# Optimization experiments

Measured on AMD Instinct MI355X. Metric: run time of the kernel, lower is better.

## Reference

```python
import jax, jax.numpy as jnp
import numpy as np
from jax import lax

B, T, C = 2, 4096, 2048
HD = 64            # args.head_size == full wkv dim here
H = 1              # num_wkv_heads (forced to 1 by time_faaaa reshape)
D = HD // H        # per-head dim
LAYER, NL = 12, 24
DMIX, DDEC = 32, 64


def setup_inputs() -> dict:
    key = jax.random.key(0)
    ks = jax.random.split(key, 12)
    r01 = LAYER / (NL - 1)          # ratio_0_to_1
    r10 = 1.0 - LAYER / NL          # ratio_1_to_almost0
    ddd = (np.arange(C, dtype=np.float64) / C)
    f32 = np.float32
    maa = lambda p: (1.0 - ddd ** p).astype(f32).reshape(1, 1, C)
    time_maa_x = jnp.asarray(maa(r10))
    time_maa_w = jnp.asarray(maa(r10))
    time_maa_k = jnp.asarray(maa(r10))
    time_maa_v = jnp.asarray((1.0 - (ddd ** r10 + 0.3 * r01)).astype(f32).reshape(1, 1, C))
    time_maa_r = jnp.asarray(maa(0.5 * r10))
    time_maa_g = jnp.asarray(maa(0.5 * r10))
    n = np.arange(HD, dtype=np.float64)
    decay_speed = (-6.0 + 5.0 * (n / (HD - 1)) ** (0.7 + 1.3 * r01)).astype(f32)
    time_decay = jnp.asarray(decay_speed.reshape(1, 1, HD))
    zig = ((np.arange(HD) + 1) % 3 - 1) * 0.1
    time_faaaa = jnp.asarray((r01 * (1.0 - n / (HD - 1)) + zig).astype(f32).reshape(H, D))
    u = lambda k, sh, s=0.01: jax.random.uniform(k, sh, jnp.float32, -s, s)
    time_maa_w1 = u(ks[0], (C, DMIX * 5))
    time_maa_w2 = u(ks[1], (5, DMIX, C))
    time_decay_w1 = u(ks[2], (C, DDEC))
    time_decay_w2 = u(ks[3], (DDEC, HD))
    W_r = jax.random.normal(ks[4], (C, HD), jnp.float32) * 0.02
    W_k = jax.random.normal(ks[5], (C, HD), jnp.float32) * 0.02
    W_v = jax.random.normal(ks[6], (C, HD), jnp.float32) * 0.02
    W_g = jax.random.normal(ks[7], (C, HD), jnp.float32) * 0.02
    W_o = jax.random.normal(ks[8], (HD, C), jnp.float32) * 0.02
    hidden_states = jax.random.normal(ks[9], (B, T, C), jnp.float32)
    shift_state = jax.random.normal(ks[10], (B, C), jnp.float32)
    wkv_state = jax.random.normal(ks[11], (B, H, D, D), jnp.float32)
    return dict(hidden_states=hidden_states, shift_state=shift_state, wkv_state=wkv_state,
                time_maa_x=time_maa_x, time_maa_w=time_maa_w, time_maa_k=time_maa_k,
                time_maa_v=time_maa_v, time_maa_r=time_maa_r, time_maa_g=time_maa_g,
                time_maa_w1=time_maa_w1, time_maa_w2=time_maa_w2,
                time_decay=time_decay, time_decay_w1=time_decay_w1, time_decay_w2=time_decay_w2,
                time_faaaa=time_faaaa, W_r=W_r, W_k=W_k, W_v=W_v, W_g=W_g, W_o=W_o)


def reference(hidden_states, shift_state, wkv_state,
              time_maa_x, time_maa_w, time_maa_k, time_maa_v, time_maa_r, time_maa_g,
              time_maa_w1, time_maa_w2, time_decay, time_decay_w1, time_decay_w2,
              time_faaaa, W_r, W_k, W_v, W_g, W_o):
    hs = hidden_states
    # token shift: prepend shift_state, drop last token, take delta
    xx = jnp.concatenate([shift_state[:, None, :], hs[:, :-1]], axis=1) - hs  # (B,T,C)
    lx = hs[:, -1]
    # LoRA token-shift mixing
    xxx = hs + xx * time_maa_x
    xxx = jnp.tanh(xxx @ time_maa_w1).reshape(B, T, 5, DMIX)
    m = jnp.einsum('btfd,fdc->fbtc', xxx, time_maa_w2)  # (5,B,T,C)
    mw, mk, mv, mr, mg = m[0], m[1], m[2], m[3], m[4]
    xw = hs + xx * (time_maa_w + mw)
    xk = hs + xx * (time_maa_k + mk)
    xv = hs + xx * (time_maa_v + mv)
    xr = hs + xx * (time_maa_r + mr)
    xg = hs + xx * (time_maa_g + mg)
    r = xr @ W_r                                  # (B,T,HD)
    k = xk @ W_k
    v = xv @ W_v
    g = jax.nn.silu(xg @ W_g)
    w = time_decay + jnp.tanh(xw @ time_decay_w1) @ time_decay_w2  # (B,T,HD)
    logw = -jnp.exp(w)                            # log of per-channel decay
    # heads: (B,T,H,D) -> time-major (T,B,H,D) for scan
    tm = lambda x: jnp.moveaxis(x.reshape(B, T, H, D), 1, 0)
    rs, ks_, vs, ws = tm(r), tm(k), tm(v), tm(logw)
    u = time_faaaa[None, :, :, None]              # (1,H,D,1) broadcast over key dim

    def step(s, inp):
        rt, kt, vt, wt = inp                      # each (B,H,D)
        kv = kt[..., :, None] * vt[..., None, :]  # (B,H,Dk,Dv)
        ot = jnp.einsum('bhk,bhkv->bhv', rt, s + u * kv)
        s = s * jnp.exp(wt)[..., None] + kv
        return s, ot

    s_final, o = lax.scan(step, wkv_state, (rs, ks_, vs, ws))
    o = jnp.moveaxis(o, 0, 1).reshape(B, T, H * D)  # (B,T,HD)
    out = (o * g) @ W_o                             # (B,T,C)
    return out, lx, s_final
```

## Files before the change

kernel.cpp:

```cpp
#include <hip/hip_runtime.h>

#define TB 2
#define TT 4096
#define TC 2048
#define TM 8192
#define THD 64
#define TNCH 64

typedef __attribute__((ext_vector_type(8))) short bf16x8;
typedef __attribute__((ext_vector_type(4))) float f32x4;

__device__ __forceinline__ float us2f(unsigned short u){
    union { unsigned int u; float f; } x; x.u = ((unsigned int)u) << 16; return x.f;
}
__device__ __forceinline__ unsigned short f2us(float f){
    unsigned int u = __float_as_uint(f);
    unsigned int r = (u + 0x7fffu + ((u >> 16) & 1u)) >> 16;
    return (unsigned short)r;
}

__global__ void k_cvt(const float* __restrict__ src, unsigned short* __restrict__ dst, int n4){
    int i = blockIdx.x * 256 + threadIdx.x;
    if (i < n4){
        float4 v = *(const float4*)(src + (size_t)i * 4);
        ushort4 u; u.x = f2us(v.x); u.y = f2us(v.y); u.z = f2us(v.z); u.w = f2us(v.w);
        *(ushort4*)(dst + (size_t)i * 4) = u;
    }
}

__global__ void k_cvt5t(const float* __restrict__ s0, const float* __restrict__ s1,
                        const float* __restrict__ s2, const float* __restrict__ s3,
                        const float* __restrict__ s4, unsigned short* __restrict__ Wblk){
    __shared__ float T[64][65];
    int tid = threadIdx.x;
    int mat = blockIdx.y, c0 = blockIdx.x * 64;
    const float* s = (mat == 0) ? s0 : (mat == 1) ? s1 : (mat == 2) ? s2 : (mat == 3) ? s3 : s4;
#pragma unroll
    for (int i = 0; i < 4; ++i){
        int idx = i * 256 + tid;
        int cc = idx >> 4, g = idx & 15;
        float4 v = *(const float4*)(s + (size_t)(c0 + cc) * 64 + g * 4);
        T[cc][g * 4 + 0] = v.x; T[cc][g * 4 + 1] = v.y;
        T[cc][g * 4 + 2] = v.z; T[cc][g * 4 + 3] = v.w;
    }
    __syncthreads();
    size_t base = ((size_t)mat * 32 + (c0 >> 6)) * 4096;
#pragma unroll
    for (int i = 0; i < 4; ++i){
        int idx = i * 256 + tid;
        int h = idx >> 4, g = idx & 15;
        ushort4 u;
        u.x = f2us(T[g * 4 + 0][h]); u.y = f2us(T[g * 4 + 1][h]);
        u.z = f2us(T[g * 4 + 2][h]); u.w = f2us(T[g * 4 + 3][h]);
        *(ushort4*)(Wblk + base + (size_t)h * 64 + g * 4) = u;
    }
}

__global__ void k_lx(const float* __restrict__ hs, float* __restrict__ o){
    int i = blockIdx.x * 256 + threadIdx.x;
    if (i < TB * TC){
        int b = i >> 11, c = i & (TC - 1);
        o[i] = hs[((size_t)(b * TT + TT - 1)) * TC + c];
    }
}

__global__ __launch_bounds__(256) void k_gemm1_mfma(
    const float* __restrict__ hs, const float* __restrict__ shift,
    const float* __restrict__ maax, const unsigned short* __restrict__ w1b,
    float* __restrict__ Gpart)
{
    __shared__ unsigned short As[64 * 40];
    __shared__ unsigned short Bs[160 * 40];
    int tid = threadIdx.x;
    int wv = tid >> 6, ln = tid & 63;
    int lm = ln & 15, lq = ln >> 4;
    int n0 = blockIdx.x * 64;
    int c0 = blockIdx.y * 256;
    f32x4 zero = {0.f, 0.f, 0.f, 0.f};
    f32x4 acc[10];
#pragma unroll
    for (int i = 0; i < 10; ++i) acc[i] = zero;

    for (int step = 0; step < 8; ++step){
        int kk0 = c0 + step * 32;
        {
            int m = tid >> 2, kg = (tid & 3) * 8;
            int n = n0 + m; int t = n & (TT - 1); int b = n >> 12;
            const float* hp = hs + (size_t)n * TC + kk0 + kg;
            const float* pp = (t == 0) ? (shift + (size_t)b * TC + kk0 + kg) : (hp - TC);
            float4 h0 = *(const float4*)hp,      h1 = *(const float4*)(hp + 4);
            float4 p0 = *(const float4*)pp,      p1 = *(const float4*)(pp + 4);
            float4 m0 = *(const float4*)(maax + kk0 + kg), m1 = *(const float4*)(maax + kk0 + kg + 4);
            ushort4 ua, ub;
            ua.x = f2us(h0.x + (p0.x - h0.x) * m0.x);
            ua.y = f2us(h0.y + (p0.y - h0.y) * m0.y);
            ua.z = f2us(h0.z + (p0.z - h0.z) * m0.z);
            ua.w = f2us(h0.w + (p0.w - h0.w) * m0.w);
            ub.x = f2us(h1.x + (p1.x - h1.x) * m1.x);
            ub.y = f2us(h1.y + (p1.y - h1.y) * m1.y);
            ub.z = f2us(h1.z + (p1.z - h1.z) * m1.z);
            ub.w = f2us(h1.w + (p1.w - h1.w) * m1.w);
            *(ushort4*)(As + m * 40 + kg) = ua;
            *(ushort4*)(As + m * 40 + kg + 4) = ub;
        }
        for (int i = tid; i < 640; i += 256){
            int k = i / 20, ng = i % 20;
            uint4 w4 = *(const uint4*)(w1b + (size_t)(kk0 + k) * 160 + ng * 8);
            const unsigned short* ww = (const unsigned short*)&w4;
#pragma unroll
            for (int j = 0; j < 8; ++j) Bs[(ng * 8 + j) * 40 + k] = ww[j];
        }
        __syncthreads();
        bf16x8 af = *(const bf16x8*)(As + (wv * 16 + lm) * 40 + lq * 8);
#pragma unroll
        for (int nt = 0; nt < 10; ++nt){
            bf16x8 bf_ = *(const bf16x8*)(Bs + (nt * 16 + lm) * 40 + lq * 8);
            acc[nt] = __builtin_amdgcn_mfma_f32_16x16x32_bf16(af, bf_, acc[nt], 0, 0, 0);
        }
        __syncthreads();
    }
    float* gp = Gpart + (size_t)blockIdx.y * TM * 160;
#pragma unroll
    for (int nt = 0; nt < 10; ++nt)
#pragma unroll
        for (int i = 0; i < 4; ++i){
            int n = n0 + wv * 16 + lq * 4 + i;
            gp[(size_t)n * 160 + nt * 16 + lm] = acc[nt][i];
        }
}

__global__ void k_g1tanhb(const float* __restrict__ Gpart, unsigned short* __restrict__ G1b){
    int i = blockIdx.x * 256 + threadIdx.x;
    if (i < 327680){
        float4 s = {0.f, 0.f, 0.f, 0.f};
        for (int kc = 0; kc < 8; ++kc){
            float4 g = *(const float4*)(Gpart + (size_t)kc * TM * 160 + (size_t)i * 4);
            s.x += g.x; s.y += g.y; s.z += g.z; s.w += g.w;
        }
        ushort4 o;
        o.x = f2us(tanhf(s.x)); o.y = f2us(tanhf(s.y));
        o.z = f2us(tanhf(s.z)); o.w = f2us(tanhf(s.w));
        *(ushort4*)(G1b + (size_t)i * 4) = o;
    }
}

__global__ __launch_bounds__(256) void k_mix_mfma(
    const float* __restrict__ hs, const float* __restrict__ shift,
    const unsigned short* __restrict__ G1b, const unsigned short* __restrict__ w2b,
    const float* __restrict__ maaw, const float* __restrict__ maak,
    const float* __restrict__ maav, const float* __restrict__ maar,
    const float* __restrict__ maag,
    unsigned short* __restrict__ X5)
{
    __shared__ unsigned short As[64 * 168];
    __shared__ unsigned short Bs[5 * 64 * 40];
    __shared__ unsigned short Xt[64 * 72];
    int tid = threadIdx.x;
    int wv = tid >> 6, ln = tid & 63;
    int lm = ln & 15, lq = ln >> 4;
    int n0 = blockIdx.x * 64, c0 = blockIdx.y * 64;

    for (int i = tid; i < 1280; i += 256){
        int r = i / 20, g = i % 20;
        uint4 v = *(const uint4*)(G1b + (size_t)(n0 + r) * 160 + g * 8);
        *(uint4*)(As + r * 168 + g * 8) = v;
    }
    for (int i = tid; i < 1280; i += 256){
        int f = i >> 8, rem = i & 255;
        int k = rem >> 3, g = rem & 7;
        uint4 w4 = *(const uint4*)(w2b + ((size_t)f * 32 + k) * TC + c0 + g * 8);
        const unsigned short* ww = (const unsigned short*)&w4;
#pragma unroll
        for (int j = 0; j < 8; ++j) Bs[f * 2560 + (g * 8 + j) * 40 + k] = ww[j];
    }
    __syncthreads();

    f32x4 zero = {0.f, 0.f, 0.f, 0.f};
    f32x4 acc[5][4];
#pragma unroll
    for (int f = 0; f < 5; ++f){
        bf16x8 af = *(const bf16x8*)(As + (wv * 16 + lm) * 168 + f * 32 + lq * 8);
#pragma unroll
        for (int nt = 0; nt < 4; ++nt){
            bf16x8 bf_ = *(const bf16x8*)(Bs + f * 2560 + (nt * 16 + lm) * 40 + lq * 8);
            acc[f][nt] = __builtin_amdgcn_mfma_f32_16x16x32_bf16(af, bf_, zero, 0, 0, 0);
        }
    }
    float hv[4][4], dv[4][4];
#pragma unroll
    for (int nt = 0; nt < 4; ++nt){
        int c = c0 + nt * 16 + lm;
#pragma unroll
        for (int i = 0; i < 4; ++i){
            int n = n0 + wv * 16 + lq * 4 + i;
            float h = hs[(size_t)n * TC + c];
            float p = ((n & (TT - 1)) == 0) ? shift[(size_t)(n >> 12) * TC + c]
                                            : hs[(size_t)(n - 1) * TC + c];
            hv[nt][i] = h; dv[nt][i] = p - h;
        }
    }
    const float* mas[5] = {maaw, maak, maav, maar, maag};
    int rr = tid >> 3, gg = tid & 7;
#pragma unroll
    for (int f = 0; f < 5; ++f){
#pragma unroll
        for (int nt = 0; nt < 4; ++nt){
            float ma = mas[f][c0 + nt * 16 + lm];
#pragma unroll
            for (int i = 0; i < 4; ++i)
                Xt[(wv * 16 + lq * 4 + i) * 72 + nt * 16 + lm] =
                    f2us(hv[nt][i] + dv[nt][i] * (ma + acc[f][nt][i]));
        }
        __syncthreads();
        unsigned short* plane = X5 + (size_t)f * TM * TC;
#pragma unroll
        for (int p = 0; p < 2; ++p){
            int r = p * 32 + rr;
            uint4 v = *(const uint4*)(Xt + r * 72 + gg * 8);
            *(uint4*)(plane + (size_t)(n0 + r) * TC + c0 + gg * 8) = v;
        }
        __syncthreads();
    }
}

__global__ __launch_bounds__(256) void k_proj_mfma(
    const unsigned short* __restrict__ X5, const unsigned short* __restrict__ Wblk,
    float* __restrict__ rbuf, float* __restrict__ kbuf, float* __restrict__ vbuf,
    float* __restrict__ gpre, float* __restrict__ dpre)
{
    __shared__ unsigned short As[2][64 * 72];
    __shared__ unsigned short Bs[2][64 * 72];
    int tid = threadIdx.x;
    int wv = tid >> 6, ln = tid & 63;
    int lm = ln & 15, lq = ln >> 4;
    int n0 = blockIdx.x * 64;
    int mat = blockIdx.y;
    int pI = (mat == 0) ? 3 : (mat == 1) ? 1 : (mat == 2) ? 2 : (mat == 3) ? 4 : 0;
    const unsigned short* A = X5 + (size_t)pI * TM * TC;
    const unsigned short* Bm = Wblk + (size_t)mat * 32 * 4096;
    float* Out = (mat == 0) ? rbuf : (mat == 1) ? kbuf : (mat == 2) ? vbuf : (mat == 3) ? gpre : dpre;

    int r0 = tid >> 3, g0 = tid & 7;
    int r1 = (tid + 256) >> 3, g1 = tid & 7;
    int lofs = r0 * 72 + g0 * 8;
    int lofs1 = r1 * 72 + g1 * 8;

    f32x4 zero = {0.f, 0.f, 0.f, 0.f};
    f32x4 acc[4];
#pragma unroll
    for (int i = 0; i < 4; ++i) acc[i] = zero;

    {
        uint4 a0 = *(const uint4*)(A + (size_t)(n0 + r0) * TC + g0 * 8);
        uint4 a1 = *(const uint4*)(A + (size_t)(n0 + r1) * TC + g1 * 8);
        uint4 b0 = *(const uint4*)(Bm + (size_t)tid * 8);
        uint4 b1 = *(const uint4*)(Bm + (size_t)(tid + 256) * 8);
        *(uint4*)(&As[0][lofs]) = a0; *(uint4*)(&As[0][lofs1]) = a1;
        *(uint4*)(&Bs[0][lofs]) = b0; *(uint4*)(&Bs[0][lofs1]) = b1;
    }
    __syncthreads();

    for (int s = 0; s < 32; ++s){
        int cur = s & 1, nxt = cur ^ 1;
        uint4 a0, a1, b0, b1;
        if (s < 31){
            int kk0 = (s + 1) * 64;
            a0 = *(const uint4*)(A + (size_t)(n0 + r0) * TC + kk0 + g0 * 8);
            a1 = *(const uint4*)(A + (size_t)(n0 + r1) * TC + kk0 + g1 * 8);
            b0 = *(const uint4*)(Bm + (size_t)(s + 1) * 4096 + (size_t)tid * 8);
            b1 = *(const uint4*)(Bm + (size_t)(s + 1) * 4096 + (size_t)(tid + 256) * 8);
        }
#pragma unroll
        for (int ks = 0; ks < 2; ++ks){
            bf16x8 af = *(const bf16x8*)(&As[cur][(wv * 16 + lm) * 72 + ks * 32 + lq * 8]);
#pragma unroll
            for (int nt = 0; nt < 4; ++nt){
                bf16x8 bw = *(const bf16x8*)(&Bs[cur][(nt * 16 + lm) * 72 + ks * 32 + lq * 8]);
                acc[nt] = __builtin_amdgcn_mfma_f32_16x16x32_bf16(af, bw, acc[nt], 0, 0, 0);
            }
        }
        if (s < 31){
            *(uint4*)(&As[nxt][lofs]) = a0; *(uint4*)(&As[nxt][lofs1]) = a1;
            *(uint4*)(&Bs[nxt][lofs]) = b0; *(uint4*)(&Bs[nxt][lofs1]) = b1;
        }
        __syncthreads();
    }
#pragma unroll
    for (int nt = 0; nt < 4; ++nt)
#pragma unroll
        for (int i = 0; i < 4; ++i){
            int n = n0 + wv * 16 + lq * 4 + i;
            Out[(size_t)n * THD + nt * 16 + lm] = acc[nt][i];
        }
}

__global__ __launch_bounds__(256) void k_wdecay(
    const float* __restrict__ dpre, const float* __restrict__ dw2,
    const float* __restrict__ tdec, float* __restrict__ logwb)
{
    __shared__ float W2s[64][65];
    __shared__ float Ths[16][65];
    int tid = threadIdx.x;
    int n0 = blockIdx.x * 16;
    for (int i = 0; i < 16; ++i){
        int flat = i * 256 + tid;
        W2s[flat >> 6][flat & 63] = dw2[flat];
    }
    for (int i = 0; i < 4; ++i){
        int flat = i * 256 + tid;
        int tt = flat >> 6, j = flat & 63;
        Ths[tt][j] = tanhf(dpre[(size_t)(n0 + tt) * THD + j]);
    }
    __syncthreads();
    int hh = tid & 63, tg = tid >> 6;
    float td = tdec[hh];
#pragma unroll
    for (int ii = 0; ii < 4; ++ii){
        int tt = tg * 4 + ii;
        float a = 0.f;
#pragma unroll 8
        for (int j = 0; j < 64; ++j) a += Ths[tt][j] * W2s[j][hh];
        logwb[(size_t)(n0 + tt) * THD + hh] = -expf(td + a);
    }
}

__global__ __launch_bounds__(256) void k_scanA(
    const float* __restrict__ kbuf, const float* __restrict__ vbuf,
    const float* __restrict__ logwb,
    float* __restrict__ chI, float* __restrict__ chP)
{
    __shared__ float kl[32][65], vl[32][65], ewl[32][65];
    int tid = threadIdx.x;
    int b = blockIdx.x >> 6, ch = blockIdx.x & 63;
    int w = tid >> 6, v = tid & 63, kb = w * 16;
    float s[16];
#pragma unroll
    for (int i = 0; i < 16; ++i) s[i] = 0.f;
    float p = 1.f;
    for (int ph = 0; ph < 2; ++ph){
        int t0 = b * TT + ch * 64 + ph * 32;
        for (int i = 0; i < 8; ++i){
            int flat = i * 256 + tid;
            int tt = flat >> 6, j = flat & 63;
            size_t g = (size_t)(t0 + tt) * THD + j;
            kl[tt][j] = kbuf[g];
            vl[tt][j] = vbuf[g];
            ewl[tt][j] = expf(logwb[g]);
        }
        __syncthreads();
        if (tid < 64){
#pragma unroll 8
            for (int t = 0; t < 32; ++t) p *= ewl[t][tid];
        }
        for (int t = 0; t < 32; ++t){
            float vv = vl[t][v];
#pragma unroll
            for (int i = 0; i < 16; ++i){
                float e = ewl[t][kb + i], kk = kl[t][kb + i];
                s[i] = s[i] * e + kk * vv;
            }
        }
        __syncthreads();
    }
    size_t base = ((size_t)(b * TNCH + ch)) * THD * THD;
#pragma unroll
    for (int i = 0; i < 16; ++i) chI[base + (size_t)(kb + i) * THD + v] = s[i];
    if (tid < 64) chP[(size_t)(b * TNCH + ch) * THD + tid] = p;
}

__global__ __launch_bounds__(256) void k_scanB(
    const float* __restrict__ chI, const float* __restrict__ chP,
    const float* __restrict__ wkv0,
    float* __restrict__ chS0, float* __restrict__ sfin)
{
    int tid = threadIdx.x;
    int blk = blockIdx.x;
    int b = blk >> 4;
    int kr = (blk & 15) * 4 + (tid >> 6);
    int v = tid & 63;
    float s = wkv0[(size_t)b * THD * THD + (size_t)kr * THD + v];
    for (int ch = 0; ch < TNCH; ++ch){
        size_t base = (size_t)(b * TNCH + ch);
        float P = chP[base * THD + kr];
        float I = chI[base * THD * THD + (size_t)kr * THD + v];
        chS0[base * THD * THD + (size_t)kr * THD + v] = s;
        s = s * P + I;
    }
    sfin[(size_t)b * THD * THD + (size_t)kr * THD + v] = s;
}

__global__ __launch_bounds__(256) void k_scanC(
    const float* __restrict__ rbuf, const float* __restrict__ kbuf,
    const float* __restrict__ vbuf, const float* __restrict__ logwb,
    const float* __restrict__ chS0, const float* __restrict__ faaaa,
    float* __restrict__ obuf)
{
    __shared__ float rl[32][65], kl[32][65], vl[32][65], ewl[32][65];
    __shared__ float part[4][64];
    __shared__ float ruk[32];
    __shared__ float ul[64];
    int tid = threadIdx.x;
    int b = blockIdx.x >> 6, ch = blockIdx.x & 63;
    int w = tid >> 6, v = tid & 63, kb = w * 16;
    if (tid < 64) ul[tid] = faaaa[tid];
    float s[16];
    {
        size_t base = ((size_t)(b * TNCH + ch)) * THD * THD;
#pragma unroll
        for (int i = 0; i < 16; ++i) s[i] = chS0[base + (size_t)(kb + i) * THD + v];
    }
    for (int ph = 0; ph < 2; ++ph){
        int t0 = b * TT + ch * 64 + ph * 32;
        for (int i = 0; i < 8; ++i){
            int flat = i * 256 + tid;
            int tt = flat >> 6, j = flat & 63;
            size_t g = (size_t)(t0 + tt) * THD + j;
            rl[tt][j] = rbuf[g];
            kl[tt][j] = kbuf[g];
            vl[tt][j] = vbuf[g];
            ewl[tt][j] = expf(logwb[g]);
        }
        __syncthreads();
        if (tid < 32){
            float a = 0.f;
#pragma unroll 8
            for (int k = 0; k < 64; ++k) a += rl[tid][k] * ul[k] * kl[tid][k];
            ruk[tid] = a;
        }
        __syncthreads();
        for (int t = 0; t < 32; ++t){
            float vv = vl[t][v];
            float pp = 0.f;
#pragma unroll
            for (int i = 0; i < 16; ++i) pp += rl[t][kb + i] * s[i];
            part[w][v] = pp;
            __syncthreads();
            if (w == 0){
                float o = part[0][v] + part[1][v] + part[2][v] + part[3][v] + ruk[t] * vv;
                obuf[(size_t)(t0 + t) * THD + v] = o;
            }
#pragma unroll
            for (int i = 0; i < 16; ++i){
                float e = ewl[t][kb + i], kk = kl[t][kb + i];
                s[i] = s[i] * e + kk * vv;
            }
            __syncthreads();
        }
    }
}

__global__ __launch_bounds__(256) void k_out_mfma(
    const float* __restrict__ obuf, const float* __restrict__ gpre,
    const unsigned short* __restrict__ Wob, float* __restrict__ outp)
{
    __shared__ unsigned short As[64 * 72];
    __shared__ unsigned short Bs[128 * 72];
    int tid = threadIdx.x;
    int wv = tid >> 6, ln = tid & 63;
    int lm = ln & 15, lq = ln >> 4;
    int n0 = blockIdx.x * 64, c0 = blockIdx.y * 128;

    for (int i = tid; i < 1024; i += 256){
        int r = i >> 4, g = i & 15;
        size_t base = (size_t)(n0 + r) * THD + g * 4;
        float4 ov = *(const float4*)(obuf + base);
        float4 gv = *(const float4*)(gpre + base);
        ushort4 u;
        u.x = f2us(ov.x * (gv.x / (1.f + expf(-gv.x))));
        u.y = f2us(ov.y * (gv.y / (1.f + expf(-gv.y))));
        u.z = f2us(ov.z * (gv.z / (1.f + expf(-gv.z))));
        u.w = f2us(ov.w * (gv.w / (1.f + expf(-gv.w))));
        *(ushort4*)(As + r * 72 + g * 4) = u;
    }
    for (int i = tid; i < 1024; i += 256){
        int k = i >> 4, ng = i & 15;
        uint4 w4 = *(const uint4*)(Wob + (size_t)k * TC + c0 + ng * 8);
        const unsigned short* ww = (const unsigned short*)&w4;
#pragma unroll
        for (int j = 0; j < 8; ++j) Bs[(ng * 8 + j) * 72 + k] = ww[j];
    }
    __syncthreads();

    f32x4 zero = {0.f, 0.f, 0.f, 0.f};
    f32x4 acc[8];
#pragma unroll
    for (int i = 0; i < 8; ++i) acc[i] = zero;
#pragma unroll
    for (int ks = 0; ks < 2; ++ks){
        bf16x8 af = *(const bf16x8*)(As + (wv * 16 + lm) * 72 + ks * 32 + lq * 8);
#pragma unroll
        for (int nt = 0; nt < 8; ++nt){
            bf16x8 bf_ = *(const bf16x8*)(Bs + (nt * 16 + lm) * 72 + ks * 32 + lq * 8);
            acc[nt] = __builtin_amdgcn_mfma_f32_16x16x32_bf16(af, bf_, acc[nt], 0, 0, 0);
        }
    }
#pragma unroll
    for (int nt = 0; nt < 8; ++nt)
#pragma unroll
        for (int i = 0; i < 4; ++i){
            int n = n0 + wv * 16 + lq * 4 + i;
            outp[(size_t)n * TC + c0 + nt * 16 + lm] = acc[nt][i];
        }
}

extern "C" void kernel_launch(void* const* d_in, const int* in_sizes, int n_in,
                              void* d_out, int out_size, void* d_ws, size_t ws_size,
                              hipStream_t stream)
{
    const float* hs    = (const float*)d_in[0];
    const float* shift = (const float*)d_in[1];
    const float* wkv0  = (const float*)d_in[2];
    const float* maax  = (const float*)d_in[3];
    const float* maaw  = (const float*)d_in[4];
    const float* maak  = (const float*)d_in[5];
    const float* maav  = (const float*)d_in[6];
    const float* maar  = (const float*)d_in[7];
    const float* maag  = (const float*)d_in[8];
    const float* w1    = (const float*)d_in[9];
    const float* w2    = (const float*)d_in[10];
    const float* tdec  = (const float*)d_in[11];
    const float* dw1   = (const float*)d_in[12];
    const float* dw2   = (const float*)d_in[13];
    const float* faaaa = (const float*)d_in[14];
    const float* Wr    = (const float*)d_in[15];
    const float* Wk    = (const float*)d_in[16];
    const float* Wv    = (const float*)d_in[17];
    const float* Wg    = (const float*)d_in[18];
    const float* Wo    = (const float*)d_in[19];

    if (ws_size < 186384384ULL) return;

    char* ws = (char*)d_ws;
    unsigned short* w1b  = (unsigned short*)(ws + 0);
    unsigned short* w2b  = (unsigned short*)(ws + 655360);
    unsigned short* Wblk = (unsigned short*)(ws + 1310720);
    unsigned short* Wob  = (unsigned short*)(ws + 2621440);
    unsigned short* G1b  = (unsigned short*)(ws + 2883584);
    char*           x5r  = ws + 8126464;
    unsigned short* X5   = (unsigned short*)x5r;
    float*          Gpart= (float*)x5r;
    float*          logwb= (float*)(x5r + 0);
    float*          obuf = (float*)(x5r + 2097152);
    float*          chI  = (float*)(x5r + 4194304);
    float*          chS0 = (float*)(x5r + 6291456);
    float*          chP  = (float*)(x5r + 8388608);
    float*          rbuf = (float*)(ws + 175898624);
    float*          kbuf = (float*)(ws + 177995776);
    float*          vbuf = (float*)(ws + 180092928);
    float*          gpre = (float*)(ws + 182190080);
    float*          dpre = (float*)(ws + 184287232);

    float* outp = (float*)d_out;
    float* lxp  = outp + (size_t)TM * TC;
    float* sfin = lxp + (size_t)TB * TC;

    k_cvt   <<<320, 256, 0, stream>>>(w1, w1b, 81920);
    k_cvt   <<<320, 256, 0, stream>>>(w2, w2b, 81920);
    k_cvt   <<<128, 256, 0, stream>>>(Wo, Wob, 32768);
    k_cvt5t <<<dim3(32, 5), 256, 0, stream>>>(Wr, Wk, Wv, Wg, dw1, Wblk);
    k_lx    <<<16, 256, 0, stream>>>(hs, lxp);

    k_gemm1_mfma <<<dim3(128, 8), 256, 0, stream>>>(hs, shift, maax, w1b, Gpart);
    k_g1tanhb    <<<1280, 256, 0, stream>>>(Gpart, G1b);
    k_mix_mfma   <<<dim3(128, 32), 256, 0, stream>>>(hs, shift, G1b, w2b,
                                                     maaw, maak, maav, maar, maag, X5);
    k_proj_mfma  <<<dim3(128, 5), 256, 0, stream>>>(X5, Wblk, rbuf, kbuf, vbuf, gpre, dpre);
    k_wdecay     <<<512, 256, 0, stream>>>(dpre, dw2, tdec, logwb);
    k_scanA      <<<128, 256, 0, stream>>>(kbuf, vbuf, logwb, chI, chP);
    k_scanB      <<<32, 256, 0, stream>>>(chI, chP, wkv0, chS0, sfin);
    k_scanC      <<<128, 256, 0, stream>>>(rbuf, kbuf, vbuf, logwb, chS0, faaaa, obuf);
    k_out_mfma   <<<dim3(128, 16), 256, 0, stream>>>(obuf, gpre, Wob, outp);
}
```

Measured before the change: 401.9 us.

## Pre-transpose w2 to bf16 and load MFMA operands directly from global in mix kernel

Adds a setup kernel that converts w2 to bf16 in a per-column transposed layout (C x 32 per mix). The mix kernel then loads its MFMA A and B fragments straight from global memory into registers instead of staging G1b and w2 tiles through shared memory with a scalar transpose and a barrier. This cuts LDS use and the uncoalesced scattered shared stores, which may raise occupancy. In exchange it adds redundant global and L2 traffic, since each wave reloads the w2 fragments. The Xt row stride also changes from 72 to 76 to alter the LDS bank mapping.

```diff
diff --git a/kernel.cpp b/kernel.cpp
--- a/kernel.cpp
+++ b/kernel.cpp
@@ -26,6 +26,29 @@
         ushort4 u; u.x = f2us(v.x); u.y = f2us(v.y); u.z = f2us(v.z); u.w = f2us(v.w);
         *(ushort4*)(dst + (size_t)i * 4) = u;
     }
+}
+
+__global__ void k_w2t(const float* __restrict__ w2, unsigned short* __restrict__ w2T){
+    __shared__ float T[32][65];
+    int tid = threadIdx.x;
+    int f = blockIdx.y, c0 = blockIdx.x * 64;
+#pragma unroll
+    for (int i = 0; i < 2; ++i){
+        int idx = i * 256 + tid;
+        int d = idx >> 4, g = idx & 15;
+        float4 v = *(const float4*)(w2 + ((size_t)f * 32 + d) * TC + c0 + g * 4);
+        T[d][g * 4 + 0] = v.x; T[d][g * 4 + 1] = v.y;
+        T[d][g * 4 + 2] = v.z; T[d][g * 4 + 3] = v.w;
+    }
+    __syncthreads();
+    int cc = tid >> 2, g = tid & 3;
+    unsigned short* dst = w2T + ((size_t)f * TC + c0 + cc) * 32 + g * 8;
+    ushort4 u0, u1;
+    u0.x = f2us(T[g * 8 + 0][cc]); u0.y = f2us(T[g * 8 + 1][cc]);
+    u0.z = f2us(T[g * 8 + 2][cc]); u0.w = f2us(T[g * 8 + 3][cc]);
+    u1.x = f2us(T[g * 8 + 4][cc]); u1.y = f2us(T[g * 8 + 5][cc]);
+    u1.z = f2us(T[g * 8 + 6][cc]); u1.w = f2us(T[g * 8 + 7][cc]);
+    *(ushort4*)dst = u0; *(ushort4*)(dst + 4) = u1;
 }
 
 __global__ void k_cvt5t(const float* __restrict__ s0, const float* __restrict__ s1,
@@ -146,46 +169,18 @@
 
 __global__ __launch_bounds__(256) void k_mix_mfma(
     const float* __restrict__ hs, const float* __restrict__ shift,
-    const unsigned short* __restrict__ G1b, const unsigned short* __restrict__ w2b,
+    const unsigned short* __restrict__ G1b, const unsigned short* __restrict__ w2T,
     const float* __restrict__ maaw, const float* __restrict__ maak,
     const float* __restrict__ maav, const float* __restrict__ maar,
     const float* __restrict__ maag,
     unsigned short* __restrict__ X5)
 {
-    __shared__ unsigned short As[64 * 168];
-    __shared__ unsigned short Bs[5 * 64 * 40];
-    __shared__ unsigned short Xt[64 * 72];
+    __shared__ unsigned short Xt[64 * 76];
     int tid = threadIdx.x;
     int wv = tid >> 6, ln = tid & 63;
     int lm = ln & 15, lq = ln >> 4;
     int n0 = blockIdx.x * 64, c0 = blockIdx.y * 64;
 
-    for (int i = tid; i < 1280; i += 256){
-        int r = i / 20, g = i % 20;
-        uint4 v = *(const uint4*)(G1b + (size_t)(n0 + r) * 160 + g * 8);
-        *(uint4*)(As + r * 168 + g * 8) = v;
-    }
-    for (int i = tid; i < 1280; i += 256){
-        int f = i >> 8, rem = i & 255;
-        int k = rem >> 3, g = rem & 7;
-        uint4 w4 = *(const uint4*)(w2b + ((size_t)f * 32 + k) * TC + c0 + g * 8);
-        const unsigned short* ww = (const unsigned short*)&w4;
-#pragma unroll
-        for (int j = 0; j < 8; ++j) Bs[f * 2560 + (g * 8 + j) * 40 + k] = ww[j];
-    }
-    __syncthreads();
-
-    f32x4 zero = {0.f, 0.f, 0.f, 0.f};
-    f32x4 acc[5][4];
-#pragma unroll
-    for (int f = 0; f < 5; ++f){
-        bf16x8 af = *(const bf16x8*)(As + (wv * 16 + lm) * 168 + f * 32 + lq * 8);
-#pragma unroll
-        for (int nt = 0; nt < 4; ++nt){
-            bf16x8 bf_ = *(const bf16x8*)(Bs + f * 2560 + (nt * 16 + lm) * 40 + lq * 8);
-            acc[f][nt] = __builtin_amdgcn_mfma_f32_16x16x32_bf16(af, bf_, zero, 0, 0, 0);
-        }
-    }
     float hv[4][4], dv[4][4];
 #pragma unroll
     for (int nt = 0; nt < 4; ++nt){
@@ -199,24 +194,38 @@
             hv[nt][i] = h; dv[nt][i] = p - h;
         }
     }
+    bf16x8 af[5];
+    {
+        const unsigned short* gp = G1b + (size_t)(n0 + wv * 16 + lm) * 160 + lq * 8;
+#pragma unroll
+        for (int f = 0; f < 5; ++f) af[f] = *(const bf16x8*)(gp + f * 32);
+    }
+    f32x4 zero = {0.f, 0.f, 0.f, 0.f};
     const float* mas[5] = {maaw, maak, maav, maar, maag};
     int rr = tid >> 3, gg = tid & 7;
 #pragma unroll
     for (int f = 0; f < 5; ++f){
+        const unsigned short* wp = w2T + ((size_t)f * TC + c0) * 32 + lq * 8;
+        f32x4 am[4];
+#pragma unroll
+        for (int nt = 0; nt < 4; ++nt){
+            bf16x8 bm = *(const bf16x8*)(wp + (size_t)(nt * 16 + lm) * 32);
+            am[nt] = __builtin_amdgcn_mfma_f32_16x16x32_bf16(af[f], bm, zero, 0, 0, 0);
+        }
 #pragma unroll
         for (int nt = 0; nt < 4; ++nt){
             float ma = mas[f][c0 + nt * 16 + lm];
 #pragma unroll
             for (int i = 0; i < 4; ++i)
-                Xt[(wv * 16 + lq * 4 + i) * 72 + nt * 16 + lm] =
-                    f2us(hv[nt][i] + dv[nt][i] * (ma + acc[f][nt][i]));
+                Xt[(wv * 16 + lq * 4 + i) * 76 + nt * 16 + lm] =
+                    f2us(hv[nt][i] + dv[nt][i] * (ma + am[nt][i]));
         }
         __syncthreads();
         unsigned short* plane = X5 + (size_t)f * TM * TC;
 #pragma unroll
         for (int p = 0; p < 2; ++p){
             int r = p * 32 + rr;
-            uint4 v = *(const uint4*)(Xt + r * 72 + gg * 8);
+            uint4 v = *(const uint4*)(Xt + r * 76 + gg * 8);
             *(uint4*)(plane + (size_t)(n0 + r) * TC + c0 + gg * 8) = v;
         }
         __syncthreads();
@@ -532,7 +541,7 @@
 
     char* ws = (char*)d_ws;
     unsigned short* w1b  = (unsigned short*)(ws + 0);
-    unsigned short* w2b  = (unsigned short*)(ws + 655360);
+    unsigned short* w2T  = (unsigned short*)(ws + 655360);
     unsigned short* Wblk = (unsigned short*)(ws + 1310720);
     unsigned short* Wob  = (unsigned short*)(ws + 2621440);
     unsigned short* G1b  = (unsigned short*)(ws + 2883584);
@@ -555,14 +564,14 @@
     float* sfin = lxp + (size_t)TB * TC;
 
     k_cvt   <<<320, 256, 0, stream>>>(w1, w1b, 81920);
-    k_cvt   <<<320, 256, 0, stream>>>(w2, w2b, 81920);
     k_cvt   <<<128, 256, 0, stream>>>(Wo, Wob, 32768);
+    k_w2t   <<<dim3(32, 5), 256, 0, stream>>>(w2, w2T);
     k_cvt5t <<<dim3(32, 5), 256, 0, stream>>>(Wr, Wk, Wv, Wg, dw1, Wblk);
     k_lx    <<<16, 256, 0, stream>>>(hs, lxp);
 
     k_gemm1_mfma <<<dim3(128, 8), 256, 0, stream>>>(hs, shift, maax, w1b, Gpart);
     k_g1tanhb    <<<1280, 256, 0, stream>>>(Gpart, G1b);
-    k_mix_mfma   <<<dim3(128, 32), 256, 0, stream>>>(hs, shift, G1b, w2b,
+    k_mix_mfma   <<<dim3(128, 32), 256, 0, stream>>>(hs, shift, G1b, w2T,
                                                      maaw, maak, maav, maar, maag, X5);
     k_proj_mfma  <<<dim3(128, 5), 256, 0, stream>>>(X5, Wblk, rbuf, kbuf, vbuf, gpre, dpre);
     k_wdecay     <<<512, 256, 0, stream>>>(dpre, dw2, tdec, logwb);
```

New measurement: 374.6 us. 6.8% less time.
